# Kernel tuning notes

Hardware: AMD Instinct MI355X
Metric: run time of the kernel (lower is better)

Reference implementation:

```python
import jax, jax.numpy as jnp
import numpy as np

TEMPERATURE = 30.0
NUM_KERNELS = 4


def setup_inputs() -> dict:
    key = jax.random.key(0)
    ks = jax.random.split(key, 7)
    B, H, W, C = 32, 56, 56, 256
    F, KH, KW, K = 256, 3, 3, NUM_KERNELS
    hidden = C // 4  # attention_reduction_ratio = 4
    x = jax.random.normal(ks[0], (B, H, W, C), dtype=jnp.float32)
    # K parallel conv kernels (HWIO layout) and biases
    fan = KH * KW * C
    kernels = jax.random.normal(ks[1], (K, KH, KW, C, F), dtype=jnp.float32) / np.sqrt(fan)
    biases = jnp.zeros((K, F), dtype=jnp.float32)
    # attention MLP: GAP -> Dense(C//4, relu) -> Dense(K)
    w1 = jax.random.normal(ks[2], (C, hidden), dtype=jnp.float32) / np.sqrt(C)
    b1 = jnp.zeros((hidden,), dtype=jnp.float32)
    w2 = jax.random.normal(ks[3], (hidden, K), dtype=jnp.float32) / np.sqrt(hidden)
    b2 = jnp.zeros((K,), dtype=jnp.float32)
    return {"x": x, "kernels": kernels, "biases": biases,
            "w1": w1, "b1": b1, "w2": w2, "b2": b2}


def reference(x, kernels, biases, w1, b1, w2, b2):
    # Attention router: GAP -> Dense(relu) -> Dense(K) -> softmax(logits / tau)
    pooled = jnp.mean(x, axis=(1, 2))                       # [B, C]
    h = jax.nn.relu(pooled @ w1 + b1)                       # [B, C//4]
    logits = h @ w2 + b2                                    # [B, K]
    attn = jax.nn.softmax(logits / TEMPERATURE, axis=-1)    # [B, K]

    # K parallel conv branches (stride 1, SAME padding, dilation 1, groups 1)
    def conv_k(w, b):
        y = jax.lax.conv_general_dilated(
            x, w, window_strides=(1, 1), padding='SAME',
            dimension_numbers=('NHWC', 'HWIO', 'NHWC'))
        return y + b                                        # [B, H, W, F]

    ys = jax.vmap(conv_k)(kernels, biases)                  # [K, B, H, W, F]
    # per-sample weighted aggregation of branch outputs
    out = jnp.einsum('kbhwf,bk->bhwf', ys, attn)            # [B, H, W, F]
    return out
```

## Files before the change

kernel.cpp:

```cpp
#include <hip/hip_runtime.h>
#include <hip/hip_bf16.h>
#include <stdint.h>

typedef __bf16 bf16_t;
typedef __bf16 bf16x4 __attribute__((ext_vector_type(4)));
typedef __bf16 bf16x8 __attribute__((ext_vector_type(8)));
typedef float floatx4 __attribute__((ext_vector_type(4)));

#define B_ 32
#define HP 58
#define WP 66

#define XPAD_OFF   0u
#define WAGG_OFF   62717952u
#define POOLED_OFF 100466688u
#define ATTN_OFF   100499456u
#define BIASAGG_OFF 100499968u

__device__ __forceinline__ void async_copy16(const void* gsrc, void* ldst) {
  __builtin_amdgcn_global_load_lds(
      (const __attribute__((address_space(1))) unsigned int*)gsrc,
      (__attribute__((address_space(3))) unsigned int*)ldst, 16, 0, 0);
}

__global__ __launch_bounds__(256)
void pad_pool(const float* __restrict__ x, bf16_t* __restrict__ xpad,
              float* __restrict__ pooled) {
  const int hp = blockIdx.x;
  const int b  = blockIdx.y;
  const int t  = threadIdx.x;
  const int c4 = (t & 63) << 2;
  const int wq = t >> 6;
  const int h  = hp - 1;
  const bool hvalid = (h >= 0) && (h < 56);
  bf16_t* dst = xpad + ((size_t)(b * 58 + hp)) * (66 * 256);
  const float* srcrow = x + ((size_t)(b * 56 + (hvalid ? h : 0))) * (56 * 256);
  floatx4 sum = {0.f, 0.f, 0.f, 0.f};
  for (int wp = wq; wp < 66; wp += 4) {
    const int w = wp - 1;
    floatx4 v = {0.f, 0.f, 0.f, 0.f};
    if (hvalid && (unsigned)w < 56u) {
      v = *(const floatx4*)(srcrow + w * 256 + c4);
      sum += v;
    }
    bf16x4 r;
#pragma unroll
    for (int j = 0; j < 4; ++j) r[j] = (bf16_t)v[j];
    *(bf16x4*)(dst + wp * 256 + c4) = r;
  }
  __shared__ floatx4 red[4][64];
  red[wq][t & 63] = sum;
  __syncthreads();
  if (hvalid && t < 64) {
    floatx4 s = red[0][t] + red[1][t] + red[2][t] + red[3][t];
#pragma unroll
    for (int j = 0; j < 4; ++j) atomicAdd(&pooled[b * 256 + t * 4 + j], s[j]);
  }
}

__global__ __launch_bounds__(256)
void router(const float* __restrict__ pooled, const float* __restrict__ w1,
            const float* __restrict__ b1, const float* __restrict__ w2,
            const float* __restrict__ b2, const float* __restrict__ biases,
            float* __restrict__ attn, float* __restrict__ biasagg) {
  __shared__ float ps[8192];
  __shared__ float w1s[16384];
  __shared__ float hs[2048];
  __shared__ float lg[128];
  __shared__ float at[128];
  const int t = threadIdx.x;
  for (int i = t; i < 8192; i += 256) ps[i] = pooled[i] * (1.0f / 3136.0f);
  for (int i = t; i < 4096; i += 256)
    *(floatx4*)&w1s[i * 4] = *(const floatx4*)&w1[i * 4];
  __syncthreads();
  for (int task = t; task < 2048; task += 256) {
    const int b = task >> 6, j = task & 63;
    const float* pb = ps + b * 256;
    float s0 = 0.f, s1 = 0.f, s2 = 0.f, s3 = 0.f;
#pragma unroll 4
    for (int c = 0; c < 256; c += 4) {
      s0 += pb[c]     * w1s[c * 64 + j];
      s1 += pb[c + 1] * w1s[(c + 1) * 64 + j];
      s2 += pb[c + 2] * w1s[(c + 2) * 64 + j];
      s3 += pb[c + 3] * w1s[(c + 3) * 64 + j];
    }
    hs[task] = fmaxf((s0 + s1) + (s2 + s3) + b1[j], 0.f);
  }
  __syncthreads();
  if (t < 128) {
    int b = t >> 2, k = t & 3;
    float s = b2[k];
    const float* hb = hs + b * 64;
#pragma unroll 4
    for (int j = 0; j < 64; ++j) s += hb[j] * w2[j * 4 + k];
    lg[t] = s * (1.0f / 30.0f);
  }
  __syncthreads();
  if (t < 32) {
    int b = t;
    float z0 = lg[b*4], z1 = lg[b*4+1], z2 = lg[b*4+2], z3 = lg[b*4+3];
    float m = fmaxf(fmaxf(z0, z1), fmaxf(z2, z3));
    float e0 = expf(z0-m), e1 = expf(z1-m), e2 = expf(z2-m), e3 = expf(z3-m);
    float inv = 1.0f / (e0 + e1 + e2 + e3);
    at[b*4] = e0*inv; at[b*4+1] = e1*inv; at[b*4+2] = e2*inv; at[b*4+3] = e3*inv;
    attn[b*4] = at[b*4]; attn[b*4+1] = at[b*4+1];
    attn[b*4+2] = at[b*4+2]; attn[b*4+3] = at[b*4+3];
  }
  __syncthreads();
  for (int i = t; i < 8192; i += 256) {
    int b = i >> 8, f = i & 255;
    biasagg[i] = at[b*4]*biases[f] + at[b*4+1]*biases[256+f]
               + at[b*4+2]*biases[512+f] + at[b*4+3]*biases[768+f];
  }
}

__global__ __launch_bounds__(256)
void wagg_kernel(const float* __restrict__ kers, const float* __restrict__ attn,
                 bf16_t* __restrict__ wagg) {
  const int lid   = blockIdx.x;
  const int xcd   = lid & 7;
  const int slice = lid >> 3;
  const int cq  = slice & 3;
  const int tap = slice >> 2;
  const int b0  = xcd << 2;
  const int t   = threadIdx.x;
  __shared__ bf16_t tile[4][64 * 260];

  float a[4][4];
#pragma unroll
  for (int i = 0; i < 4; ++i)
#pragma unroll
    for (int k = 0; k < 4; ++k) a[i][k] = attn[(b0 + i) * 4 + k];

  const float* k0 = kers + ((size_t)(0 * 9 + tap)) * 65536;
  const float* k1 = kers + ((size_t)(1 * 9 + tap)) * 65536;
  const float* k2 = kers + ((size_t)(2 * 9 + tap)) * 65536;
  const float* k3 = kers + ((size_t)(3 * 9 + tap)) * 65536;

  const int fq = t & 63;
  const int cl = t >> 6;
  const int f0 = fq * 4;
#pragma unroll
  for (int pass = 0; pass < 16; ++pass) {
    const int c_local = pass * 4 + cl;
    const size_t o = (size_t)(cq * 64 + c_local) * 256 + f0;
    floatx4 v0 = *(const floatx4*)(k0 + o);
    floatx4 v1 = *(const floatx4*)(k1 + o);
    floatx4 v2 = *(const floatx4*)(k2 + o);
    floatx4 v3 = *(const floatx4*)(k3 + o);
#pragma unroll
    for (int i = 0; i < 4; ++i) {
      bf16x4 r;
#pragma unroll
      for (int j = 0; j < 4; ++j)
        r[j] = (bf16_t)(a[i][0] * v0[j] + a[i][1] * v1[j] + a[i][2] * v2[j] + a[i][3] * v3[j]);
      *(bf16x4*)&tile[i][c_local * 260 + f0] = r;
    }
  }
  __syncthreads();

#pragma unroll
  for (int i = 0; i < 4; ++i) {
    bf16_t* wt = wagg + ((size_t)((b0 + i) * 9 + tap)) * 65536 + cq * 64;
#pragma unroll
    for (int pass = 0; pass < 8; ++pass) {
      const int gi = pass * 256 + t;
      const int f  = gi >> 3;
      const int cg = gi & 7;
      bf16x8 v;
#pragma unroll
      for (int jj = 0; jj < 8; ++jj) v[jj] = tile[i][(cg * 8 + jj) * 260 + f];
      *(bf16x8*)(wt + (size_t)f * 256 + cg * 8) = v;
    }
  }
}

#define PBUF_BYTES 20480
#define BBUF_BYTES 16384

__global__ __launch_bounds__(256, 2)
void conv_mfma(const bf16_t* __restrict__ xpad, const bf16_t* __restrict__ wagg,
               const float* __restrict__ biasagg, float* __restrict__ out) {
  __shared__ char lds[PBUF_BYTES + 3 * BBUF_BYTES];
  char* ldsP = lds;
  char* ldsB = lds + PBUF_BYTES;

  const int lid  = blockIdx.y * 28 + blockIdx.x;
  const int nid  = (lid & 7) * 112 + (lid >> 3);
  const int b    = nid / 28;
  const int tile = nid - b * 28;
  const int h0 = (tile >> 2) * 8;
  const int w0 = (tile & 3) * 14;

  const int tid  = threadIdx.x;
  const int lane = tid & 63;
  const int wv   = tid >> 6;
  const int l15  = lane & 15;
  const int quad = lane >> 4;
  const int n0   = wv * 64;

  const char* xb = (const char*)xpad + (size_t)b * (HP * WP * 256 * 2);
  const char* wb = (const char*)wagg + (size_t)b * (9 * 256 * 256 * 2);

  int offs[7];
#pragma unroll
  for (int mi = 0; mi < 7; ++mi) {
    int m = mi * 16 + l15;
    int ty = m / 14;
    int tx = m - ty * 14;
    offs[mi] = ty * 16 + tx;
  }
  int boff[4];
#pragma unroll
  for (int ni = 0; ni < 4; ++ni) {
    int f = n0 + ni * 16 + l15;
    boff[ni] = f * 64 + ((quad ^ ((f >> 1) & 3)) << 4);
  }

  floatx4 acc[7][4];
#pragma unroll
  for (int mi = 0; mi < 7; ++mi)
#pragma unroll
    for (int ni = 0; ni < 4; ++ni) acc[mi][ni] = (floatx4){0.f, 0.f, 0.f, 0.f};

  auto stage_patch = [&](int cq) {
#pragma unroll
    for (int ii = 0; ii < 5; ++ii) {
      int i20 = wv * 5 + ii;
      int p = i20 * 8 + (lane >> 3);
      int gsrc = (lane & 7) ^ (p & 7);
      const char* src = xb + ((size_t)((h0 + (p >> 4)) * WP + (w0 + (p & 15))) * 512)
                           + cq * 128 + gsrc * 16;
      async_copy16(src, ldsP + i20 * 1024);
    }
  };
  auto stage_b = [&](int cq, int tap, int ks, int slot) {
    const char* wt = wb + (size_t)tap * (256 * 256 * 2);
    int kbyte = cq * 128 + ks * 64;
#pragma unroll
    for (int ii = 0; ii < 4; ++ii) {
      int i16 = wv * 4 + ii;
      int f = i16 * 16 + (lane >> 2);
      int gsrc = (lane & 3) ^ ((f >> 1) & 3);
      const char* src = wt + f * 512 + kbyte + gsrc * 16;
      async_copy16(src, ldsB + slot * BBUF_BYTES + i16 * 1024);
    }
  };

  stage_patch(0);
  stage_b(0, 0, 0, 0);

  int cq = 0, tap = 0, ks = 0;
  int bcur = 0, bnxt = 1;
  while (true) {
    int nks = ks + 1, ntap = tap, ncq = cq;
    if (nks == 2) { nks = 0; ++ntap; if (ntap == 9) { ntap = 0; ++ncq; } }
    const bool have_next = (ncq < 4);
    if (have_next) {
      stage_b(ncq, ntap, nks, bnxt);
      asm volatile("s_waitcnt vmcnt(4)" ::: "memory");
    } else {
      asm volatile("s_waitcnt vmcnt(0)" ::: "memory");
    }
    __builtin_amdgcn_s_barrier();
    __builtin_amdgcn_sched_barrier(0);
    {
      const char* pc = ldsP;
      const char* bc = ldsB + bcur * BBUF_BYTES;
      const int tapoff = (tap / 3) * 16 + (tap % 3);
      const int gA = ks * 4 + quad;
      bf16x8 a[7];
#pragma unroll
      for (int mi = 0; mi < 7; ++mi) {
        int p = offs[mi] + tapoff;
        int addr = (p << 7) + ((gA ^ (p & 7)) << 4);
        a[mi] = *(const bf16x8*)(pc + addr);
      }
      bf16x8 bv[4];
#pragma unroll
      for (int ni = 0; ni < 4; ++ni) bv[ni] = *(const bf16x8*)(bc + boff[ni]);
#pragma unroll
      for (int mi = 0; mi < 7; ++mi)
#pragma unroll
        for (int ni = 0; ni < 4; ++ni)
          acc[mi][ni] = __builtin_amdgcn_mfma_f32_16x16x32_bf16(a[mi], bv[ni], acc[mi][ni], 0, 0, 0);
    }
    if (!have_next) break;
    if (ncq != cq) {
      __builtin_amdgcn_s_barrier();
      stage_patch(ncq);
    }
    cq = ncq; tap = ntap; ks = nks;
    bcur = bnxt; bnxt = bnxt + 1; if (bnxt == 3) bnxt = 0;
  }

  float bias[4];
#pragma unroll
  for (int ni = 0; ni < 4; ++ni) bias[ni] = biasagg[b * 256 + n0 + ni * 16 + l15];
  float* outb = out + (size_t)b * (56 * 56 * 256);
#pragma unroll
  for (int mi = 0; mi < 7; ++mi) {
#pragma unroll
    for (int rg = 0; rg < 4; ++rg) {
      int m = mi * 16 + quad * 4 + rg;
      int ty = m / 14, tx = m - ty * 14;
      float* orow = outb + ((size_t)((h0 + ty) * 56) + (w0 + tx)) * 256 + n0 + l15;
#pragma unroll
      for (int ni = 0; ni < 4; ++ni) orow[ni * 16] = acc[mi][ni][rg] + bias[ni];
    }
  }
}

extern "C" void kernel_launch(void* const* d_in, const int* in_sizes, int n_in,
                              void* d_out, int out_size, void* d_ws, size_t ws_size,
                              hipStream_t stream) {
  const float* x      = (const float*)d_in[0];
  const float* kers   = (const float*)d_in[1];
  const float* biases = (const float*)d_in[2];
  const float* w1     = (const float*)d_in[3];
  const float* b1     = (const float*)d_in[4];
  const float* w2     = (const float*)d_in[5];
  const float* b2     = (const float*)d_in[6];
  float* outp = (float*)d_out;
  char* ws = (char*)d_ws;

  bf16_t* xpad   = (bf16_t*)(ws + XPAD_OFF);
  bf16_t* wagg   = (bf16_t*)(ws + WAGG_OFF);
  float* pooled  = (float*)(ws + POOLED_OFF);
  float* attn    = (float*)(ws + ATTN_OFF);
  float* biasagg = (float*)(ws + BIASAGG_OFF);

  hipMemsetAsync(pooled, 0, 32 * 256 * sizeof(float), stream);
  pad_pool<<<dim3(58, 32), 256, 0, stream>>>(x, xpad, pooled);
  router<<<1, 256, 0, stream>>>(pooled, w1, b1, w2, b2, biases, attn, biasagg);
  wagg_kernel<<<dim3(288), 256, 0, stream>>>(kers, attn, wagg);
  conv_mfma<<<dim3(28, 32), 256, 0, stream>>>(xpad, wagg, biasagg, outp);
}
```

Before: 381.4 us.

## Software-pipeline conv A-fragment loads and split wagg into finer slices

The conv main loop now processes both k-halves of a tap in one iteration. It preloads the next tap's A fragments from LDS right after the current MFMAs, and derives the second-half A addresses by XOR. Staging addresses are precomputed once, and MFMA sections run at raised wave priority via s_setprio. The wagg kernel is split into twice as many blocks, each handling 32 channels with half the LDS tile, to improve parallelism. The aim is to hide LDS latency and address arithmetic behind MFMA, at the cost of more live registers (aA/aB), which could pressure occupancy at two blocks per CU.

```diff
diff --git a/kernel.cpp b/kernel.cpp
--- a/kernel.cpp
+++ b/kernel.cpp
@@ -117,14 +117,14 @@
 __global__ __launch_bounds__(256)
 void wagg_kernel(const float* __restrict__ kers, const float* __restrict__ attn,
                  bf16_t* __restrict__ wagg) {
-  const int lid   = blockIdx.x;
-  const int xcd   = lid & 7;
-  const int slice = lid >> 3;
-  const int cq  = slice & 3;
-  const int tap = slice >> 2;
+  const int lid = blockIdx.x;
+  const int xcd = lid & 7;
+  const int sl  = lid >> 3;
+  const int c8  = sl & 7;
+  const int tap = sl >> 3;
   const int b0  = xcd << 2;
   const int t   = threadIdx.x;
-  __shared__ bf16_t tile[4][64 * 260];
+  __shared__ bf16_t tile[4][32 * 260];
 
   float a[4][4];
 #pragma unroll
@@ -132,18 +132,18 @@
 #pragma unroll
     for (int k = 0; k < 4; ++k) a[i][k] = attn[(b0 + i) * 4 + k];
 
-  const float* k0 = kers + ((size_t)(0 * 9 + tap)) * 65536;
-  const float* k1 = kers + ((size_t)(1 * 9 + tap)) * 65536;
-  const float* k2 = kers + ((size_t)(2 * 9 + tap)) * 65536;
-  const float* k3 = kers + ((size_t)(3 * 9 + tap)) * 65536;
+  const float* k0 = kers + ((size_t)(0 * 9 + tap)) * 65536 + (size_t)(c8 * 32) * 256;
+  const float* k1 = kers + ((size_t)(1 * 9 + tap)) * 65536 + (size_t)(c8 * 32) * 256;
+  const float* k2 = kers + ((size_t)(2 * 9 + tap)) * 65536 + (size_t)(c8 * 32) * 256;
+  const float* k3 = kers + ((size_t)(3 * 9 + tap)) * 65536 + (size_t)(c8 * 32) * 256;
 
   const int fq = t & 63;
   const int cl = t >> 6;
   const int f0 = fq * 4;
 #pragma unroll
-  for (int pass = 0; pass < 16; ++pass) {
+  for (int pass = 0; pass < 8; ++pass) {
     const int c_local = pass * 4 + cl;
-    const size_t o = (size_t)(cq * 64 + c_local) * 256 + f0;
+    const size_t o = (size_t)c_local * 256 + f0;
     floatx4 v0 = *(const floatx4*)(k0 + o);
     floatx4 v1 = *(const floatx4*)(k1 + o);
     floatx4 v2 = *(const floatx4*)(k2 + o);
@@ -161,12 +161,12 @@
 
 #pragma unroll
   for (int i = 0; i < 4; ++i) {
-    bf16_t* wt = wagg + ((size_t)((b0 + i) * 9 + tap)) * 65536 + cq * 64;
-#pragma unroll
-    for (int pass = 0; pass < 8; ++pass) {
+    bf16_t* wt = wagg + ((size_t)((b0 + i) * 9 + tap)) * 65536 + c8 * 32;
+#pragma unroll
+    for (int pass = 0; pass < 4; ++pass) {
       const int gi = pass * 256 + t;
-      const int f  = gi >> 3;
-      const int cg = gi & 7;
+      const int f  = gi >> 2;
+      const int cg = gi & 3;
       bf16x8 v;
 #pragma unroll
       for (int jj = 0; jj < 8; ++jj) v[jj] = tile[i][(cg * 8 + jj) * 260 + f];
@@ -216,6 +216,24 @@
     int f = n0 + ni * 16 + l15;
     boff[ni] = f * 64 + ((quad ^ ((f >> 1) & 3)) << 4);
   }
+  int sb_off[4], sb_lds[4];
+#pragma unroll
+  for (int ii = 0; ii < 4; ++ii) {
+    int i16 = wv * 4 + ii;
+    int f = i16 * 16 + (lane >> 2);
+    int gsrc = (lane & 3) ^ ((f >> 1) & 3);
+    sb_off[ii] = f * 512 + gsrc * 16;
+    sb_lds[ii] = i16 * 1024;
+  }
+  int sp_off[5], sp_lds[5];
+#pragma unroll
+  for (int ii = 0; ii < 5; ++ii) {
+    int i20 = wv * 5 + ii;
+    int p = i20 * 8 + (lane >> 3);
+    int gsrc = (lane & 7) ^ (p & 7);
+    sp_off[ii] = ((h0 + (p >> 4)) * WP + (w0 + (p & 15))) * 512 + gsrc * 16;
+    sp_lds[ii] = i20 * 1024;
+  }
 
   floatx4 acc[7][4];
 #pragma unroll
@@ -225,39 +243,68 @@
 
   auto stage_patch = [&](int cq) {
 #pragma unroll
-    for (int ii = 0; ii < 5; ++ii) {
-      int i20 = wv * 5 + ii;
-      int p = i20 * 8 + (lane >> 3);
-      int gsrc = (lane & 7) ^ (p & 7);
-      const char* src = xb + ((size_t)((h0 + (p >> 4)) * WP + (w0 + (p & 15))) * 512)
-                           + cq * 128 + gsrc * 16;
-      async_copy16(src, ldsP + i20 * 1024);
-    }
+    for (int ii = 0; ii < 5; ++ii)
+      async_copy16(xb + cq * 128 + sp_off[ii], ldsP + sp_lds[ii]);
   };
-  auto stage_b = [&](int cq, int tap, int ks, int slot) {
-    const char* wt = wb + (size_t)tap * (256 * 256 * 2);
-    int kbyte = cq * 128 + ks * 64;
-#pragma unroll
-    for (int ii = 0; ii < 4; ++ii) {
-      int i16 = wv * 4 + ii;
-      int f = i16 * 16 + (lane >> 2);
-      int gsrc = (lane & 3) ^ ((f >> 1) & 3);
-      const char* src = wt + f * 512 + kbyte + gsrc * 16;
-      async_copy16(src, ldsB + slot * BBUF_BYTES + i16 * 1024);
-    }
+  auto stage_b = [&](int tap, int kbyte, int slot) {
+    const char* wtb = wb + (size_t)tap * 131072 + kbyte;
+#pragma unroll
+    for (int ii = 0; ii < 4; ++ii)
+      async_copy16(wtb + sb_off[ii], ldsB + slot * BBUF_BYTES + sb_lds[ii]);
   };
 
   stage_patch(0);
-  stage_b(0, 0, 0, 0);
-
-  int cq = 0, tap = 0, ks = 0;
-  int bcur = 0, bnxt = 1;
-  while (true) {
-    int nks = ks + 1, ntap = tap, ncq = cq;
-    if (nks == 2) { nks = 0; ++ntap; if (ntap == 9) { ntap = 0; ++ncq; } }
-    const bool have_next = (ncq < 4);
-    if (have_next) {
-      stage_b(ncq, ntap, nks, bnxt);
+  stage_b(0, 0, 0);
+
+  bf16x8 aA[7], aB[7];
+  int aoff[7];
+  int slot = 0;
+
+#pragma unroll 1
+  for (int d = 0; d < 36; ++d) {
+    const int cq  = d / 9;
+    const int tap = d - cq * 9;
+    const int s1 = (slot == 2) ? 0 : slot + 1;
+    const int s2 = (s1 == 2) ? 0 : s1 + 1;
+
+    stage_b(tap, cq * 128 + 64, s1);
+    asm volatile("s_waitcnt vmcnt(4)" ::: "memory");
+    __builtin_amdgcn_s_barrier();
+    __builtin_amdgcn_sched_barrier(0);
+    {
+      const char* bc = ldsB + slot * BBUF_BYTES;
+      bf16x8 bv0 = *(const bf16x8*)(bc + boff[0]);
+      bf16x8 bv1 = *(const bf16x8*)(bc + boff[1]);
+      bf16x8 bv2 = *(const bf16x8*)(bc + boff[2]);
+      bf16x8 bv3 = *(const bf16x8*)(bc + boff[3]);
+      if (tap == 0) {
+        const int tapoff = 0;
+#pragma unroll
+        for (int mi = 0; mi < 7; ++mi) {
+          int p = offs[mi] + tapoff;
+          aoff[mi] = (p << 7) + ((quad ^ (p & 7)) << 4);
+          aA[mi] = *(const bf16x8*)(ldsP + aoff[mi]);
+        }
+      }
+#pragma unroll
+      for (int mi = 0; mi < 7; ++mi)
+        aB[mi] = *(const bf16x8*)(ldsP + (aoff[mi] ^ 64));
+      __builtin_amdgcn_s_setprio(1);
+#pragma unroll
+      for (int mi = 0; mi < 7; ++mi) {
+        acc[mi][0] = __builtin_amdgcn_mfma_f32_16x16x32_bf16(aA[mi], bv0, acc[mi][0], 0, 0, 0);
+        acc[mi][1] = __builtin_amdgcn_mfma_f32_16x16x32_bf16(aA[mi], bv1, acc[mi][1], 0, 0, 0);
+        acc[mi][2] = __builtin_amdgcn_mfma_f32_16x16x32_bf16(aA[mi], bv2, acc[mi][2], 0, 0, 0);
+        acc[mi][3] = __builtin_amdgcn_mfma_f32_16x16x32_bf16(aA[mi], bv3, acc[mi][3], 0, 0, 0);
+      }
+      __builtin_amdgcn_s_setprio(0);
+    }
+
+    const bool last = (d == 35);
+    if (!last) {
+      const int ntap = (tap == 8) ? 0 : tap + 1;
+      const int ncq  = (tap == 8) ? cq + 1 : cq;
+      stage_b(ntap, ncq * 128, s2);
       asm volatile("s_waitcnt vmcnt(4)" ::: "memory");
     } else {
       asm volatile("s_waitcnt vmcnt(0)" ::: "memory");
@@ -265,33 +312,34 @@
     __builtin_amdgcn_s_barrier();
     __builtin_amdgcn_sched_barrier(0);
     {
-      const char* pc = ldsP;
-      const char* bc = ldsB + bcur * BBUF_BYTES;
-      const int tapoff = (tap / 3) * 16 + (tap % 3);
-      const int gA = ks * 4 + quad;
-      bf16x8 a[7];
+      const char* bc = ldsB + s1 * BBUF_BYTES;
+      bf16x8 bv0 = *(const bf16x8*)(bc + boff[0]);
+      bf16x8 bv1 = *(const bf16x8*)(bc + boff[1]);
+      bf16x8 bv2 = *(const bf16x8*)(bc + boff[2]);
+      bf16x8 bv3 = *(const bf16x8*)(bc + boff[3]);
+      __builtin_amdgcn_s_setprio(1);
 #pragma unroll
       for (int mi = 0; mi < 7; ++mi) {
-        int p = offs[mi] + tapoff;
-        int addr = (p << 7) + ((gA ^ (p & 7)) << 4);
-        a[mi] = *(const bf16x8*)(pc + addr);
+        acc[mi][0] = __builtin_amdgcn_mfma_f32_16x16x32_bf16(aB[mi], bv0, acc[mi][0], 0, 0, 0);
+        acc[mi][1] = __builtin_amdgcn_mfma_f32_16x16x32_bf16(aB[mi], bv1, acc[mi][1], 0, 0, 0);
+        acc[mi][2] = __builtin_amdgcn_mfma_f32_16x16x32_bf16(aB[mi], bv2, acc[mi][2], 0, 0, 0);
+        acc[mi][3] = __builtin_amdgcn_mfma_f32_16x16x32_bf16(aB[mi], bv3, acc[mi][3], 0, 0, 0);
       }
-      bf16x8 bv[4];
-#pragma unroll
-      for (int ni = 0; ni < 4; ++ni) bv[ni] = *(const bf16x8*)(bc + boff[ni]);
-#pragma unroll
-      for (int mi = 0; mi < 7; ++mi)
-#pragma unroll
-        for (int ni = 0; ni < 4; ++ni)
-          acc[mi][ni] = __builtin_amdgcn_mfma_f32_16x16x32_bf16(a[mi], bv[ni], acc[mi][ni], 0, 0, 0);
-    }
-    if (!have_next) break;
-    if (ncq != cq) {
-      __builtin_amdgcn_s_barrier();
-      stage_patch(ncq);
-    }
-    cq = ncq; tap = ntap; ks = nks;
-    bcur = bnxt; bnxt = bnxt + 1; if (bnxt == 3) bnxt = 0;
+      __builtin_amdgcn_s_setprio(0);
+      if (tap < 8) {
+        const int ntapoff = ((tap + 1) / 3) * 16 + ((tap + 1) % 3);
+#pragma unroll
+        for (int mi = 0; mi < 7; ++mi) {
+          int p = offs[mi] + ntapoff;
+          aoff[mi] = (p << 7) + ((quad ^ (p & 7)) << 4);
+          aA[mi] = *(const bf16x8*)(ldsP + aoff[mi]);
+        }
+      } else if (!last) {
+        __builtin_amdgcn_s_barrier();
+        stage_patch(cq + 1);
+      }
+    }
+    slot = s2;
   }
 
   float bias[4];
@@ -333,6 +381,6 @@
   hipMemsetAsync(pooled, 0, 32 * 256 * sizeof(float), stream);
   pad_pool<<<dim3(58, 32), 256, 0, stream>>>(x, xpad, pooled);
   router<<<1, 256, 0, stream>>>(pooled, w1, b1, w2, b2, biases, attn, biasagg);
-  wagg_kernel<<<dim3(288), 256, 0, stream>>>(kers, attn, wagg);
+  wagg_kernel<<<dim3(576), 256, 0, stream>>>(kers, attn, wagg);
   conv_mfma<<<dim3(28, 32), 256, 0, stream>>>(xpad, wagg, biasagg, outp);
 }
```

New measurement: 371.7 us. -2.5%, faster.
